# Optimization experiments

Measured on AMD Instinct MI355X. Metric: run time of the kernel, lower is better.

Reference implementation:

```python
import jax, jax.numpy as jnp
import numpy as np

N = 50000   # num nodes
E = 400000  # num edges (avg degree 8)
D = 256     # in_channels
H = 256     # hidden_channels
C = 64      # out_channels
K = 2       # k_hops


def setup_inputs() -> dict:
    key = jax.random.key(0)
    ks = jax.random.split(key, 10)
    x = jax.random.normal(ks[0], (N, D), dtype=jnp.float32)
    edge_index = jax.random.randint(ks[1], (2, E), 0, N, dtype=jnp.int32)
    s = 0.05
    # per-hop linears of the single H2GCNConv (weights stored [in, out])
    W0 = jax.random.normal(ks[2], (D, H), jnp.float32) * s
    W1 = jax.random.normal(ks[3], (D, H), jnp.float32) * s
    W2 = jax.random.normal(ks[4], (D, H), jnp.float32) * s
    b0 = jnp.zeros((H,), jnp.float32)
    b1 = jnp.zeros((H,), jnp.float32)
    b2 = jnp.zeros((H,), jnp.float32)
    # classifier: h2_out_dim = H*(K+1) = 768 -> C
    Wc = jax.random.normal(ks[5], (H * (K + 1), C), jnp.float32) * s
    bc = jnp.zeros((C,), jnp.float32)
    return {"x": x, "edge_index": edge_index, "num_nodes": N,
            "W0": W0, "b0": b0, "W1": W1, "b1": b1, "W2": W2, "b2": b2,
            "Wc": Wc, "bc": bc}


def _normalize_adj(edge_index, num_nodes):
    # add self loops, then D^{-1/2} A D^{-1/2} edge weights
    loops = jnp.arange(num_nodes, dtype=edge_index.dtype)
    ei = jnp.concatenate([edge_index, jnp.stack([loops, loops])], axis=1)
    row, col = ei[0], ei[1]
    deg = jax.ops.segment_sum(jnp.ones(row.shape[0], jnp.float32), row,
                              num_segments=num_nodes)
    dis = jnp.where(deg > 0, deg ** -0.5, 0.0)  # inf -> 0 for isolated nodes
    return ei, dis[row] * dis[col]


def _sparse_mm(edge_index, edge_weight, x, num_nodes):
    # gather -> scale -> scatter-add (COO SpMM)
    row, col = edge_index[0], edge_index[1]
    msg = x[col] * edge_weight[:, None]  # [E', F]
    return jax.ops.segment_sum(msg, row, num_segments=num_nodes)


def reference(x, edge_index, num_nodes, W0, b0, W1, b1, W2, b2, Wc, bc):
    ei, ew = _normalize_adj(edge_index, num_nodes)
    # H2GCNConv: ego + k-hop aggregates, each through its own linear, concat
    outs = [x @ W0 + b0]
    cur = x
    for Wk, bk in ((W1, b1), (W2, b2)):
        cur = _sparse_mm(ei, ew, cur, num_nodes)
        outs.append(cur @ Wk + bk)
    h = jax.nn.relu(jnp.concatenate(outs, axis=1))  # [N, 3H]
    # dropout p=0 / eval mode -> identity
    return h @ Wc + bc
```

## Files before the change

### kernel.cpp

```cpp
#include <hip/hip_runtime.h>


#define FD 256
#define CO 64
#define SB 512
#define MT1 391
#define PS (50048 * 256)

using frag_ab = __attribute__((ext_vector_type(8))) short;
using f32x4   = __attribute__((ext_vector_type(4))) float;
typedef unsigned short u16;
typedef unsigned int   u32;

__device__ __forceinline__ u16 f2bf(float f) {
    u32 u = __builtin_bit_cast(u32, f);
    return (u16)((u + 0x7FFFu + ((u >> 16) & 1u)) >> 16);
}
__device__ __forceinline__ float bfl(u32 packed) {
    return __builtin_bit_cast(float, packed << 16);
}
__device__ __forceinline__ float bfh(u32 packed) {
    return __builtin_bit_cast(float, packed & 0xFFFF0000u);
}

__device__ __forceinline__ void gll16(const void* g, void* l) {
    __builtin_amdgcn_global_load_lds(
        (const __attribute__((address_space(1))) u32*)g,
        (__attribute__((address_space(3))) u32*)l, 16, 0, 0);
}

#define BAR()  __builtin_amdgcn_s_barrier()
#define WLG0() asm volatile("s_waitcnt lgkmcnt(0)" ::: "memory")
#define WVM0() asm volatile("s_waitcnt vmcnt(0)" ::: "memory")
#define WVM2() asm volatile("s_waitcnt vmcnt(2)" ::: "memory")

__global__ void zerok(int4* __restrict__ deg4, int4* __restrict__ fill4, int n4) {
    int i = blockIdx.x * blockDim.x + threadIdx.x;
    int4 z = make_int4(0, 0, 0, 0);
    if (i < n4) { deg4[i] = z; fill4[i] = z; }
}
__global__ void count_kernel(const int* __restrict__ ei0, int* deg, int e) {
    int i = blockIdx.x * blockDim.x + threadIdx.x;
    if (i < e) atomicAdd(&deg[ei0[i]], 1);
}
__global__ void scan1(const int* __restrict__ deg, int* __restrict__ rowptr,
                      int* __restrict__ bsum, float* __restrict__ dis, int n) {
    __shared__ int sh[SB];
    int tid = threadIdx.x;
    int i = blockIdx.x * SB + tid;
    int v = (i < n) ? deg[i] + 1 : 0;
    if (i < n) dis[i] = rsqrtf((float)v);
    sh[tid] = v;
    __syncthreads();
    for (int off = 1; off < SB; off <<= 1) {
        int add = (tid >= off) ? sh[tid - off] : 0;
        __syncthreads();
        sh[tid] += add;
        __syncthreads();
    }
    if (i < n) rowptr[i] = sh[tid] - v;
    if (tid == SB - 1) bsum[blockIdx.x] = sh[tid];
}
__global__ void scan2(const int* __restrict__ bsum, int* __restrict__ bscan, int nb) {
    __shared__ int sh[128];
    int tid = threadIdx.x;
    int v = (tid < nb) ? bsum[tid] : 0;
    sh[tid] = v;
    __syncthreads();
    for (int off = 1; off < 128; off <<= 1) {
        int add = (tid >= off) ? sh[tid - off] : 0;
        __syncthreads();
        sh[tid] += add;
        __syncthreads();
    }
    if (tid < nb) bscan[tid] = sh[tid] - v;
    if (tid == nb - 1) bscan[nb] = sh[tid];
}
__global__ void scan3(int* rowptr, const int* __restrict__ bscan, int n, int nb) {
    int i = blockIdx.x * 256 + threadIdx.x;
    if (i < n) rowptr[i] += bscan[i / SB];
    if (i == n) rowptr[n] = bscan[nb];
}
__global__ void fill_kernel(const int* __restrict__ ei, const float* __restrict__ dis,
                            const int* __restrict__ rowptr, int* fill,
                            int2* __restrict__ cw, int e, int n) {
    int i = blockIdx.x * blockDim.x + threadIdx.x;
    if (i >= e + n) return;
    int r, c;
    if (i < e) { r = ei[i]; c = ei[e + i]; }
    else       { r = i - e; c = r; }
    float w = dis[r] * dis[c];
    int pos = rowptr[r] + atomicAdd(&fill[r], 1);
    int2 p; p.x = c; p.y = __float_as_int(w);
    cw[pos] = p;
}

__global__ void conv_kernel(const float* __restrict__ x, u16* __restrict__ xb, int total4) {
    int i = blockIdx.x * blockDim.x + threadIdx.x;
    if (i < total4) {
        float4 v = ((const float4*)x)[i];
        ushort4 o;
        o.x = f2bf(v.x); o.y = f2bf(v.y); o.z = f2bf(v.z); o.w = f2bf(v.w);
        ((ushort4*)xb)[i] = o;
    }
}
__global__ void wtrans_kernel(const float* __restrict__ W0, const float* __restrict__ W1,
                              const float* __restrict__ W2, const float* __restrict__ Wc,
                              u16* __restrict__ WkT, u16* __restrict__ WcT) {
    __shared__ u16 tl[64][65];
    int b = blockIdx.x;
    const float* src; u16* dst; int R, C, r0, c0;
    if (b < 48) {
        int k = b >> 4, t = b & 15;
        src = (k == 0) ? W0 : (k == 1) ? W1 : W2;
        dst = WkT + k * 65536;
        R = 256; C = 256; r0 = (t >> 2) * 64; c0 = (t & 3) * 64;
    } else {
        int t = b - 48;
        src = Wc; dst = WcT;
        R = 768; C = 64; r0 = t * 64; c0 = 0;
    }
    int tid = threadIdx.x;
    int rr = tid >> 4, cc = (tid & 15) * 4;
    #pragma unroll
    for (int it = 0; it < 4; ++it) {
        int r = it * 16 + rr;
        float4 v = *(const float4*)(src + (size_t)(r0 + r) * C + c0 + cc);
        tl[cc + 0][r] = f2bf(v.x); tl[cc + 1][r] = f2bf(v.y);
        tl[cc + 2][r] = f2bf(v.z); tl[cc + 3][r] = f2bf(v.w);
    }
    __syncthreads();
    #pragma unroll
    for (int it = 0; it < 4; ++it) {
        int crow = it * 16 + rr;
        ushort4 o;
        o.x = tl[crow][cc + 0]; o.y = tl[crow][cc + 1];
        o.z = tl[crow][cc + 2]; o.w = tl[crow][cc + 3];
        *(ushort4*)(dst + (size_t)(c0 + crow) * R + r0 + cc) = o;
    }
}

__global__ void spmm_bf16(const int* __restrict__ rowptr, const int2* __restrict__ cw,
                          const u16* __restrict__ xb, u16* __restrict__ outb, int n) {
    int tid = threadIdx.x;
    int lane = tid & 63;
    int row = blockIdx.x * 8 + ((tid >> 6) << 1) + (lane >> 5);
    if (row >= n) return;
    int l32 = lane & 31;
    int p0 = rowptr[row], p1 = rowptr[row + 1];
    float a[8];
    #pragma unroll
    for (int j = 0; j < 8; ++j) a[j] = 0.f;

    int p = p0;
    for (; p + 8 <= p1; p += 8) {
        int2 cwv[8]; uint4 v[8];
        #pragma unroll
        for (int u = 0; u < 8; ++u) cwv[u] = cw[p + u];
        #pragma unroll
        for (int u = 0; u < 8; ++u)
            v[u] = *(const uint4*)(xb + (size_t)cwv[u].x * FD + l32 * 8);
        #pragma unroll
        for (int u = 0; u < 8; ++u) {
            float wt = __int_as_float(cwv[u].y);
            a[0] += wt * bfl(v[u].x); a[1] += wt * bfh(v[u].x);
            a[2] += wt * bfl(v[u].y); a[3] += wt * bfh(v[u].y);
            a[4] += wt * bfl(v[u].z); a[5] += wt * bfh(v[u].z);
            a[6] += wt * bfl(v[u].w); a[7] += wt * bfh(v[u].w);
        }
    }
    for (; p + 2 <= p1; p += 2) {
        int2 cwv[2]; uint4 v[2];
        #pragma unroll
        for (int u = 0; u < 2; ++u) cwv[u] = cw[p + u];
        #pragma unroll
        for (int u = 0; u < 2; ++u)
            v[u] = *(const uint4*)(xb + (size_t)cwv[u].x * FD + l32 * 8);
        #pragma unroll
        for (int u = 0; u < 2; ++u) {
            float wt = __int_as_float(cwv[u].y);
            a[0] += wt * bfl(v[u].x); a[1] += wt * bfh(v[u].x);
            a[2] += wt * bfl(v[u].y); a[3] += wt * bfh(v[u].y);
            a[4] += wt * bfl(v[u].z); a[5] += wt * bfh(v[u].z);
            a[6] += wt * bfl(v[u].w); a[7] += wt * bfh(v[u].w);
        }
    }
    for (; p < p1; ++p) {
        int2 cwv = cw[p];
        float wt = __int_as_float(cwv.y);
        uint4 v = *(const uint4*)(xb + (size_t)cwv.x * FD + l32 * 8);
        a[0] += wt * bfl(v.x); a[1] += wt * bfh(v.x);
        a[2] += wt * bfl(v.y); a[3] += wt * bfh(v.y);
        a[4] += wt * bfl(v.z); a[5] += wt * bfh(v.z);
        a[6] += wt * bfl(v.w); a[7] += wt * bfh(v.w);
    }
    uint4 o;
    o.x = (u32)f2bf(a[0]) | ((u32)f2bf(a[1]) << 16);
    o.y = (u32)f2bf(a[2]) | ((u32)f2bf(a[3]) << 16);
    o.z = (u32)f2bf(a[4]) | ((u32)f2bf(a[5]) << 16);
    o.w = (u32)f2bf(a[6]) | ((u32)f2bf(a[7]) << 16);
    *(uint4*)(outb + (size_t)row * FD + l32 * 8) = o;
}

__launch_bounds__(256, 4)
__global__ void gemm1(const u16* __restrict__ xb, const u16* __restrict__ agg1b,
                      const u16* __restrict__ agg2b, const u16* __restrict__ WkT,
                      const float* __restrict__ b0, const float* __restrict__ b1,
                      const float* __restrict__ b2, u16* __restrict__ T, int n) {
    __shared__ __align__(16) char lds[32768];

    const int tid = threadIdx.x;
    const int w = tid >> 6, l = tid & 63;
    const int l4 = l >> 4, lm = l & 15;
    const int mq = w & 1, nq = w >> 1;

    int nwg = gridDim.x;
    int q8 = nwg >> 3, r8 = nwg & 7;
    int xcd = blockIdx.x & 7, idx = blockIdx.x >> 3;
    int bid = (xcd < r8 ? xcd * (q8 + 1) : r8 * (q8 + 1) + (xcd - r8) * q8) + idx;

    const int nt  = bid & 1;
    int rest = bid >> 1;
    const int mt  = rest % MT1;
    const int seg = rest / MT1;
    const int row0 = mt * 128;
    const int n0   = nt * 128;

    const u16* inb = (seg == 0) ? xb : (seg == 1) ? agg1b : agg2b;
    const u16* WT  = WkT + (size_t)seg * 65536;
    const float* bk = (seg == 0) ? b0 : (seg == 1) ? b1 : b2;

    auto stage = [&](int kt, char* buf) {
        #pragma unroll
        for (int i = 0; i < 2; ++i) {
            int L = w * 1024 + i * 4096 + l * 16;
            int r = L >> 6, s = (L >> 4) & 3;
            int k16 = s ^ (r & 3);
            int gr = row0 + r; if (gr > n - 1) gr = n - 1;
            gll16(inb + (size_t)gr * FD + kt * 32 + k16 * 8, buf + w * 1024 + i * 4096);
        }
        #pragma unroll
        for (int i = 0; i < 2; ++i) {
            int L = w * 1024 + i * 4096 + l * 16;
            int r = L >> 6, s = (L >> 4) & 3;
            int k16 = s ^ (r & 3);
            gll16(WT + (size_t)(n0 + r) * FD + kt * 32 + k16 * 8,
                  buf + 8192 + w * 1024 + i * 4096);
        }
    };

    f32x4 acc[4][4];
    #pragma unroll
    for (int jm = 0; jm < 4; ++jm)
        #pragma unroll
        for (int rn = 0; rn < 4; ++rn) acc[jm][rn] = (f32x4)(0.f);

    stage(0, lds);
    WVM0();
    BAR();

    #pragma unroll
    for (int kt = 0; kt < 8; ++kt) {
        char* cur = lds + (kt & 1) * 16384;
        if (kt < 7) stage(kt + 1, lds + ((kt + 1) & 1) * 16384);

        frag_ab af[4], bf_[4];
        #pragma unroll
        for (int jm = 0; jm < 4; ++jm) {
            int rB = nq * 64 + jm * 16 + lm;
            af[jm] = *(const frag_ab*)(cur + 8192 + rB * 64 + ((l4 ^ (rB & 3)) << 4));
        }
        #pragma unroll
        for (int rn = 0; rn < 4; ++rn) {
            int rA = mq * 64 + rn * 16 + lm;
            bf_[rn] = *(const frag_ab*)(cur + rA * 64 + ((l4 ^ (rA & 3)) << 4));
        }
        #pragma unroll
        for (int jm = 0; jm < 4; ++jm)
            #pragma unroll
            for (int rn = 0; rn < 4; ++rn)
                acc[jm][rn] = __builtin_amdgcn_mfma_f32_16x16x32_bf16(af[jm], bf_[rn], acc[jm][rn], 0, 0, 0);

        if (kt < 7) WVM0();
        WLG0();
        BAR();
    }

    #pragma unroll
    for (int jm = 0; jm < 4; ++jm) {
        int j = nq * 64 + jm * 16 + l4 * 4;
        float4 bb = *(const float4*)(bk + n0 + j);
        #pragma unroll
        for (int rn = 0; rn < 4; ++rn) {
            int r = mq * 64 + rn * 16 + lm;
            f32x4 v = acc[jm][rn];
            ushort4 p;
            p.x = f2bf(fmaxf(v[0] + bb.x, 0.f));
            p.y = f2bf(fmaxf(v[1] + bb.y, 0.f));
            p.z = f2bf(fmaxf(v[2] + bb.z, 0.f));
            p.w = f2bf(fmaxf(v[3] + bb.w, 0.f));
            *(ushort4*)(lds + r * 256 + (((j >> 3) ^ (r & 7)) << 4) + (j & 7) * 2) = p;
        }
    }
    WLG0();
    BAR();

    u16* Tp = T + (size_t)seg * PS;
    {
        const int c16 = tid & 15;
        #pragma unroll
        for (int i = 0; i < 8; ++i) {
            int r = i * 16 + (tid >> 4);
            uint4 v = *(const uint4*)(lds + r * 256 + ((c16 ^ (r & 7)) << 4));
            *(uint4*)(Tp + (size_t)(row0 + r) * FD + n0 + c16 * 8) = v;
        }
    }
}

__launch_bounds__(256, 3)
__global__ void gemm2(const u16* __restrict__ T, const u16* __restrict__ WcT,
                      const float* __restrict__ bc, float* __restrict__ out, int n) {
    __shared__ __align__(16) char lds[16384];
    const int tid = threadIdx.x;
    const int w = tid >> 6, l = tid & 63;
    const int l4 = l >> 4, lm = l & 15;
    const int row0 = blockIdx.x * 64;
    const int rr = w * 16 + lm;
    const int r  = row0 + rr;

    frag_ab b[24];
    #pragma unroll
    for (int kt = 0; kt < 12; ++kt)
        #pragma unroll
        for (int kk2 = 0; kk2 < 2; ++kk2)
            b[kt * 2 + kk2] = *(const frag_ab*)(T + (size_t)(kt >> 2) * PS +
                                                (size_t)r * FD + (kt & 3) * 64 + kk2 * 32 + l4 * 8);

    auto stageW = [&](int kt, char* buf) {
        #pragma unroll
        for (int i = 0; i < 2; ++i) {
            int L = tid * 16 + i * 4096;
            int c = L >> 7, s = (L >> 4) & 7;
            gll16(WcT + (size_t)c * 768 + kt * 64 + (s ^ (c & 7)) * 8,
                  buf + w * 1024 + i * 4096);
        }
    };

    f32x4 acc[4];
    #pragma unroll
    for (int am = 0; am < 4; ++am) acc[am] = (f32x4)(0.f);

    stageW(0, lds);
    #pragma unroll
    for (int kt = 0; kt < 12; ++kt) {
        char* cur = lds + (kt & 1) * 8192;
        if (kt < 11) {
            stageW(kt + 1, lds + ((kt + 1) & 1) * 8192);
            WVM2();
        } else {
            WVM0();
        }
        BAR();
        #pragma unroll
        for (int kk2 = 0; kk2 < 2; ++kk2) {
            #pragma unroll
            for (int am = 0; am < 4; ++am) {
                int c = am * 16 + lm;
                frag_ab afr = *(const frag_ab*)(cur + c * 128 + (((kk2 * 4 + l4) ^ (c & 7)) << 4));
                acc[am] = __builtin_amdgcn_mfma_f32_16x16x32_bf16(afr, b[kt * 2 + kk2], acc[am], 0, 0, 0);
            }
        }
        WLG0();
        BAR();
    }

    if (r < n) {
        #pragma unroll
        for (int am = 0; am < 4; ++am) {
            float4 bb = *(const float4*)(bc + am * 16 + l4 * 4);
            float4 o;
            o.x = acc[am][0] + bb.x;
            o.y = acc[am][1] + bb.y;
            o.z = acc[am][2] + bb.z;
            o.w = acc[am][3] + bb.w;
            *(float4*)(out + (size_t)r * CO + am * 16 + l4 * 4) = o;
        }
    }
}

extern "C" void kernel_launch(void* const* d_in, const int* in_sizes, int n_in,
                              void* d_out, int out_size, void* d_ws, size_t ws_size,
                              hipStream_t stream) {
    const float* x  = (const float*)d_in[0];
    const int*   ei = (const int*)d_in[1];
    const float* W0 = (const float*)d_in[3];
    const float* b0 = (const float*)d_in[4];
    const float* W1 = (const float*)d_in[5];
    const float* b1 = (const float*)d_in[6];
    const float* W2 = (const float*)d_in[7];
    const float* b2 = (const float*)d_in[8];
    const float* Wc = (const float*)d_in[9];
    const float* bc = (const float*)d_in[10];
    float* out = (float*)d_out;

    const int n  = in_sizes[0] / FD;
    const int e  = in_sizes[1] / 2;
    const int ep = e + n;
    const int nb = (n + SB - 1) / SB;

    char* ws = (char*)d_ws;
    size_t o = 0;
    auto take = [&](size_t nbytes) -> char* {
        char* p = ws + o;
        o += (nbytes + 255) & ~(size_t)255;
        return p;
    };
    int*   deg    = (int*)  take((size_t)n * 4);
    int*   fill   = (int*)  take((size_t)n * 4);
    float* dis    = (float*)take((size_t)n * 4);
    int*   rowptr = (int*)  take((size_t)(n + 1) * 4);
    int*   bsum   = (int*)  take((size_t)(nb + 1) * 4);
    int*   bscan  = (int*)  take((size_t)(nb + 1) * 4);
    int2*  cw     = (int2*) take((size_t)ep * 8);
    u16*   xb     = (u16*)  take((size_t)n * FD * 2);
    u16*   agg1b  = (u16*)  take((size_t)n * FD * 2);
    u16*   agg2b  = (u16*)  take((size_t)n * FD * 2);
    u16*   WkT    = (u16*)  take((size_t)3 * FD * FD * 2);
    u16*   WcT    = (u16*)  take((size_t)CO * 3 * FD * 2);
    u16*   T      = (u16*)  take((size_t)3 * PS * 2);
    (void)ws_size; (void)n_in; (void)out_size;

    const int n4 = (n + 3) / 4;
    zerok       <<<(n4 + 255) / 256, 256, 0, stream>>>((int4*)deg, (int4*)fill, n4);
    count_kernel<<<(e + 255) / 256, 256, 0, stream>>>(ei, deg, e);
    scan1       <<<nb, SB, 0, stream>>>(deg, rowptr, bsum, dis, n);
    scan2       <<<1, 128, 0, stream>>>(bsum, bscan, nb);
    scan3       <<<(n + 256) / 256, 256, 0, stream>>>(rowptr, bscan, n, nb);
    fill_kernel <<<(ep + 255) / 256, 256, 0, stream>>>(ei, dis, rowptr, fill, cw, e, n);

    const int total4 = n * FD / 4;
    conv_kernel  <<<(total4 + 255) / 256, 256, 0, stream>>>(x, xb, total4);
    wtrans_kernel<<<60, 256, 0, stream>>>(W0, W1, W2, Wc, WkT, WcT);

    spmm_bf16<<<(n + 7) / 8, 256, 0, stream>>>(rowptr, cw, xb, agg1b, n);
    spmm_bf16<<<(n + 7) / 8, 256, 0, stream>>>(rowptr, cw, agg1b, agg2b, n);

    gemm1<<<2 * MT1 * 3, 256, 0, stream>>>(xb, agg1b, agg2b, WkT, b0, b1, b2, T, n);
    gemm2<<<(n + 63) / 64, 256, 0, stream>>>(T, WcT, bc, out, n);
}
```

Before: 204.0 us.

## Fuse per-hop GEMMs and classifier GEMM, keeping hidden tile in LDS

Replaces the two GEMM kernels with one kernel where each 64-row block computes the three per-hop 256-wide linears plus ReLU, stores the bf16 hidden tile in shared memory, and immediately multiplies it by the matching slice of the classifier weights. This removes the write and re-read of the large intermediate T buffer in global memory and one kernel launch. In exchange each block uses 72KB of LDS at lower occupancy (launch bounds 2). Every block also re-streams the full 256x256 hop weights for a smaller 64-row tile, so weight traffic per output row rises.

```diff
diff --git a/kernel.cpp b/kernel.cpp
--- a/kernel.cpp
+++ b/kernel.cpp
@@ -4,8 +4,6 @@
 #define FD 256
 #define CO 64
 #define SB 512
-#define MT1 391
-#define PS (50048 * 256)
 
 using frag_ab = __attribute__((ext_vector_type(8))) short;
 using f32x4   = __attribute__((ext_vector_type(4))) float;
@@ -202,188 +200,152 @@
     *(uint4*)(outb + (size_t)row * FD + l32 * 8) = o;
 }
 
-__launch_bounds__(256, 4)
-__global__ void gemm1(const u16* __restrict__ xb, const u16* __restrict__ agg1b,
-                      const u16* __restrict__ agg2b, const u16* __restrict__ WkT,
-                      const float* __restrict__ b0, const float* __restrict__ b1,
-                      const float* __restrict__ b2, u16* __restrict__ T, int n) {
-    __shared__ __align__(16) char lds[32768];
-
-    const int tid = threadIdx.x;
-    const int w = tid >> 6, l = tid & 63;
-    const int l4 = l >> 4, lm = l & 15;
-    const int mq = w & 1, nq = w >> 1;
-
-    int nwg = gridDim.x;
-    int q8 = nwg >> 3, r8 = nwg & 7;
-    int xcd = blockIdx.x & 7, idx = blockIdx.x >> 3;
-    int bid = (xcd < r8 ? xcd * (q8 + 1) : r8 * (q8 + 1) + (xcd - r8) * q8) + idx;
-
-    const int nt  = bid & 1;
-    int rest = bid >> 1;
-    const int mt  = rest % MT1;
-    const int seg = rest / MT1;
-    const int row0 = mt * 128;
-    const int n0   = nt * 128;
-
-    const u16* inb = (seg == 0) ? xb : (seg == 1) ? agg1b : agg2b;
-    const u16* WT  = WkT + (size_t)seg * 65536;
-    const float* bk = (seg == 0) ? b0 : (seg == 1) ? b1 : b2;
-
-    auto stage = [&](int kt, char* buf) {
-        #pragma unroll
-        for (int i = 0; i < 2; ++i) {
-            int L = w * 1024 + i * 4096 + l * 16;
-            int r = L >> 6, s = (L >> 4) & 3;
-            int k16 = s ^ (r & 3);
-            int gr = row0 + r; if (gr > n - 1) gr = n - 1;
-            gll16(inb + (size_t)gr * FD + kt * 32 + k16 * 8, buf + w * 1024 + i * 4096);
-        }
-        #pragma unroll
-        for (int i = 0; i < 2; ++i) {
-            int L = w * 1024 + i * 4096 + l * 16;
-            int r = L >> 6, s = (L >> 4) & 3;
-            int k16 = s ^ (r & 3);
-            gll16(WT + (size_t)(n0 + r) * FD + kt * 32 + k16 * 8,
-                  buf + 8192 + w * 1024 + i * 4096);
-        }
-    };
-
-    f32x4 acc[4][4];
-    #pragma unroll
-    for (int jm = 0; jm < 4; ++jm)
-        #pragma unroll
-        for (int rn = 0; rn < 4; ++rn) acc[jm][rn] = (f32x4)(0.f);
-
-    stage(0, lds);
-    WVM0();
-    BAR();
-
-    #pragma unroll
-    for (int kt = 0; kt < 8; ++kt) {
-        char* cur = lds + (kt & 1) * 16384;
-        if (kt < 7) stage(kt + 1, lds + ((kt + 1) & 1) * 16384);
-
-        frag_ab af[4], bf_[4];
-        #pragma unroll
-        for (int jm = 0; jm < 4; ++jm) {
-            int rB = nq * 64 + jm * 16 + lm;
-            af[jm] = *(const frag_ab*)(cur + 8192 + rB * 64 + ((l4 ^ (rB & 3)) << 4));
-        }
-        #pragma unroll
-        for (int rn = 0; rn < 4; ++rn) {
-            int rA = mq * 64 + rn * 16 + lm;
-            bf_[rn] = *(const frag_ab*)(cur + rA * 64 + ((l4 ^ (rA & 3)) << 4));
-        }
-        #pragma unroll
-        for (int jm = 0; jm < 4; ++jm)
-            #pragma unroll
-            for (int rn = 0; rn < 4; ++rn)
-                acc[jm][rn] = __builtin_amdgcn_mfma_f32_16x16x32_bf16(af[jm], bf_[rn], acc[jm][rn], 0, 0, 0);
-
-        if (kt < 7) WVM0();
-        WLG0();
-        BAR();
-    }
-
-    #pragma unroll
-    for (int jm = 0; jm < 4; ++jm) {
-        int j = nq * 64 + jm * 16 + l4 * 4;
-        float4 bb = *(const float4*)(bk + n0 + j);
-        #pragma unroll
-        for (int rn = 0; rn < 4; ++rn) {
-            int r = mq * 64 + rn * 16 + lm;
-            f32x4 v = acc[jm][rn];
-            ushort4 p;
-            p.x = f2bf(fmaxf(v[0] + bb.x, 0.f));
-            p.y = f2bf(fmaxf(v[1] + bb.y, 0.f));
-            p.z = f2bf(fmaxf(v[2] + bb.z, 0.f));
-            p.w = f2bf(fmaxf(v[3] + bb.w, 0.f));
-            *(ushort4*)(lds + r * 256 + (((j >> 3) ^ (r & 7)) << 4) + (j & 7) * 2) = p;
-        }
-    }
-    WLG0();
-    BAR();
-
-    u16* Tp = T + (size_t)seg * PS;
-    {
-        const int c16 = tid & 15;
-        #pragma unroll
-        for (int i = 0; i < 8; ++i) {
-            int r = i * 16 + (tid >> 4);
-            uint4 v = *(const uint4*)(lds + r * 256 + ((c16 ^ (r & 7)) << 4));
-            *(uint4*)(Tp + (size_t)(row0 + r) * FD + n0 + c16 * 8) = v;
-        }
-    }
-}
-
-__launch_bounds__(256, 3)
-__global__ void gemm2(const u16* __restrict__ T, const u16* __restrict__ WcT,
-                      const float* __restrict__ bc, float* __restrict__ out, int n) {
-    __shared__ __align__(16) char lds[16384];
+__launch_bounds__(256, 2)
+__global__ void fused_gemm(const u16* __restrict__ xb, const u16* __restrict__ agg1b,
+                           const u16* __restrict__ agg2b, const u16* __restrict__ WkT,
+                           const float* __restrict__ b0, const float* __restrict__ b1,
+                           const float* __restrict__ b2, const u16* __restrict__ WcT,
+                           const float* __restrict__ bc, float* __restrict__ out, int n) {
+    __shared__ __align__(16) char lds[73728];
+    char* Tl = lds + 40960;
+
     const int tid = threadIdx.x;
     const int w = tid >> 6, l = tid & 63;
     const int l4 = l >> 4, lm = l & 15;
     const int row0 = blockIdx.x * 64;
     const int rr = w * 16 + lm;
-    const int r  = row0 + rr;
-
-    frag_ab b[24];
+
+    f32x4 oacc[4];
     #pragma unroll
-    for (int kt = 0; kt < 12; ++kt)
-        #pragma unroll
-        for (int kk2 = 0; kk2 < 2; ++kk2)
-            b[kt * 2 + kk2] = *(const frag_ab*)(T + (size_t)(kt >> 2) * PS +
-                                                (size_t)r * FD + (kt & 3) * 64 + kk2 * 32 + l4 * 8);
-
-    auto stageW = [&](int kt, char* buf) {
-        #pragma unroll
-        for (int i = 0; i < 2; ++i) {
-            int L = tid * 16 + i * 4096;
-            int c = L >> 7, s = (L >> 4) & 7;
-            gll16(WcT + (size_t)c * 768 + kt * 64 + (s ^ (c & 7)) * 8,
-                  buf + w * 1024 + i * 4096);
-        }
-    };
-
-    f32x4 acc[4];
-    #pragma unroll
-    for (int am = 0; am < 4; ++am) acc[am] = (f32x4)(0.f);
-
-    stageW(0, lds);
-    #pragma unroll
-    for (int kt = 0; kt < 12; ++kt) {
-        char* cur = lds + (kt & 1) * 8192;
-        if (kt < 11) {
-            stageW(kt + 1, lds + ((kt + 1) & 1) * 8192);
-            WVM2();
-        } else {
-            WVM0();
-        }
+    for (int am = 0; am < 4; ++am) oacc[am] = (f32x4)(0.f);
+
+    for (int seg = 0; seg < 3; ++seg) {
+        const u16* inb = (seg == 0) ? xb : (seg == 1) ? agg1b : agg2b;
+        const u16* WT  = WkT + (size_t)seg * 65536;
+        const float* bk = (seg == 0) ? b0 : (seg == 1) ? b1 : b2;
+
+        auto stageB = [&](int kt, int pb) {
+            {
+                int L = tid * 16;
+                int r = L >> 6, s = (L >> 4) & 3;
+                int gr = row0 + r; if (gr > n - 1) gr = n - 1;
+                gll16(inb + (size_t)gr * FD + kt * 32 + (s ^ (r & 3)) * 8,
+                      lds + pb * 4096 + L);
+            }
+            #pragma unroll
+            for (int i = 0; i < 4; ++i) {
+                int L = tid * 16 + i * 4096;
+                int j = L >> 6, s = (L >> 4) & 3;
+                gll16(WT + (size_t)j * FD + kt * 32 + (s ^ (j & 3)) * 8,
+                      lds + 8192 + pb * 16384 + L);
+            }
+        };
+
+        f32x4 acc[4][4];
+        #pragma unroll
+        for (int jm = 0; jm < 4; ++jm)
+            #pragma unroll
+            for (int rn = 0; rn < 4; ++rn) acc[jm][rn] = (f32x4)(0.f);
+
+        stageB(0, 0);
+        WVM0();
         BAR();
-        #pragma unroll
-        for (int kk2 = 0; kk2 < 2; ++kk2) {
-            #pragma unroll
-            for (int am = 0; am < 4; ++am) {
-                int c = am * 16 + lm;
-                frag_ab afr = *(const frag_ab*)(cur + c * 128 + (((kk2 * 4 + l4) ^ (c & 7)) << 4));
-                acc[am] = __builtin_amdgcn_mfma_f32_16x16x32_bf16(afr, b[kt * 2 + kk2], acc[am], 0, 0, 0);
+
+        #pragma unroll
+        for (int kt = 0; kt < 8; ++kt) {
+            char* curA = lds + (kt & 1) * 4096;
+            char* curW = lds + 8192 + (kt & 1) * 16384;
+            if (kt < 7) stageB(kt + 1, (kt + 1) & 1);
+
+            frag_ab af[4], bf_[4];
+            #pragma unroll
+            for (int jm = 0; jm < 4; ++jm) {
+                int j = w * 64 + jm * 16 + lm;
+                af[jm] = *(const frag_ab*)(curW + j * 64 + ((l4 ^ (j & 3)) << 4));
+            }
+            #pragma unroll
+            for (int rn = 0; rn < 4; ++rn) {
+                int r = rn * 16 + lm;
+                bf_[rn] = *(const frag_ab*)(curA + r * 64 + ((l4 ^ (r & 3)) << 4));
+            }
+            #pragma unroll
+            for (int jm = 0; jm < 4; ++jm)
+                #pragma unroll
+                for (int rn = 0; rn < 4; ++rn)
+                    acc[jm][rn] = __builtin_amdgcn_mfma_f32_16x16x32_bf16(af[jm], bf_[rn], acc[jm][rn], 0, 0, 0);
+
+            if (kt < 7) WVM0();
+            WLG0();
+            BAR();
+        }
+
+        auto stageC = [&](int kt2, int pb) {
+            #pragma unroll
+            for (int i = 0; i < 2; ++i) {
+                int L = tid * 16 + i * 4096;
+                int c = L >> 7, s = (L >> 4) & 7;
+                gll16(WcT + (size_t)c * 768 + seg * 256 + kt2 * 64 + (s ^ (c & 7)) * 8,
+                      lds + 8192 + pb * 8192 + L);
+            }
+        };
+        stageC(0, 0);
+
+        #pragma unroll
+        for (int jm = 0; jm < 4; ++jm) {
+            int j0 = w * 64 + jm * 16 + l4 * 4;
+            float4 bb = *(const float4*)(bk + j0);
+            #pragma unroll
+            for (int rn = 0; rn < 4; ++rn) {
+                int r = rn * 16 + lm;
+                f32x4 v = acc[jm][rn];
+                ushort4 p;
+                p.x = f2bf(fmaxf(v[0] + bb.x, 0.f));
+                p.y = f2bf(fmaxf(v[1] + bb.y, 0.f));
+                p.z = f2bf(fmaxf(v[2] + bb.z, 0.f));
+                p.w = f2bf(fmaxf(v[3] + bb.w, 0.f));
+                *(ushort4*)(Tl + r * 512 + (((j0 >> 3) ^ (r & 7)) << 4) + (j0 & 7) * 2) = p;
             }
         }
         WLG0();
         BAR();
-    }
-
-    if (r < n) {
+
+        #pragma unroll
+        for (int kt2 = 0; kt2 < 4; ++kt2) {
+            char* cw_ = lds + 8192 + (kt2 & 1) * 8192;
+            if (kt2 < 3) {
+                stageC(kt2 + 1, (kt2 + 1) & 1);
+                WVM2();
+            } else {
+                WVM0();
+            }
+            BAR();
+            #pragma unroll
+            for (int kk2 = 0; kk2 < 2; ++kk2) {
+                int g = kt2 * 8 + kk2 * 4 + l4;
+                frag_ab bfr = *(const frag_ab*)(Tl + rr * 512 + ((g ^ (rr & 7)) << 4));
+                #pragma unroll
+                for (int am = 0; am < 4; ++am) {
+                    int c = am * 16 + lm;
+                    frag_ab afr = *(const frag_ab*)(cw_ + c * 128 + (((kk2 * 4 + l4) ^ (c & 7)) << 4));
+                    oacc[am] = __builtin_amdgcn_mfma_f32_16x16x32_bf16(afr, bfr, oacc[am], 0, 0, 0);
+                }
+            }
+            WLG0();
+            BAR();
+        }
+    }
+
+    int gr = row0 + rr;
+    if (gr < n) {
         #pragma unroll
         for (int am = 0; am < 4; ++am) {
             float4 bb = *(const float4*)(bc + am * 16 + l4 * 4);
             float4 o;
-            o.x = acc[am][0] + bb.x;
-            o.y = acc[am][1] + bb.y;
-            o.z = acc[am][2] + bb.z;
-            o.w = acc[am][3] + bb.w;
-            *(float4*)(out + (size_t)r * CO + am * 16 + l4 * 4) = o;
+            o.x = oacc[am][0] + bb.x;
+            o.y = oacc[am][1] + bb.y;
+            o.z = oacc[am][2] + bb.z;
+            o.w = oacc[am][3] + bb.w;
+            *(float4*)(out + (size_t)gr * CO + am * 16 + l4 * 4) = o;
         }
     }
 }
@@ -427,7 +389,6 @@
     u16*   agg2b  = (u16*)  take((size_t)n * FD * 2);
     u16*   WkT    = (u16*)  take((size_t)3 * FD * FD * 2);
     u16*   WcT    = (u16*)  take((size_t)CO * 3 * FD * 2);
-    u16*   T      = (u16*)  take((size_t)3 * PS * 2);
     (void)ws_size; (void)n_in; (void)out_size;
 
     const int n4 = (n + 3) / 4;
@@ -445,6 +406,6 @@
     spmm_bf16<<<(n + 7) / 8, 256, 0, stream>>>(rowptr, cw, xb, agg1b, n);
     spmm_bf16<<<(n + 7) / 8, 256, 0, stream>>>(rowptr, cw, agg1b, agg2b, n);
 
-    gemm1<<<2 * MT1 * 3, 256, 0, stream>>>(xb, agg1b, agg2b, WkT, b0, b1, b2, T, n);
-    gemm2<<<(n + 63) / 64, 256, 0, stream>>>(T, WcT, bc, out, n);
-}
+    fused_gemm<<<(n + 63) / 64, 256, 0, stream>>>(xb, agg1b, agg2b, WkT,
+                                                  b0, b1, b2, WcT, bc, out, n);
+}
```

New measurement: 197.3 us. 3.3% less time.
